# Kernel tuning notes

Measured on AMD Instinct MI355X. Metric: run time of the kernel, lower is better.

Reference implementation:

```python
import jax, jax.numpy as jnp
import numpy as np
import math

D, H, S, B, E, FF = 768, 12, 1024, 2, 32768, 4 * 768
HD = D // H


def layer_norm(x, g, b, eps=1e-5):
    m = jnp.mean(x, axis=-1, keepdims=True)
    v = jnp.mean((x - m) ** 2, axis=-1, keepdims=True)
    return (x - m) / jnp.sqrt(v + eps) * g + b


def setup_inputs() -> dict:
    key = jax.random.key(0)
    ks = jax.random.split(key, 24)
    w = lambda k, shape: jax.random.normal(k, shape, dtype=jnp.float32) * 0.02
    inp = {
        "x": jax.random.normal(ks[0], (B, S, D), dtype=jnp.float32),
        "adj_mask": jax.random.randint(ks[1], (B, S, S), 0, 2).astype(bool),
        "edge_attr": jax.random.normal(ks[2], (E,), dtype=jnp.float32),
        "edge_index": jax.random.randint(ks[3], (2, E), 0, S),
        "norm1_g": jnp.ones((D,), jnp.float32),
        "norm1_b": jnp.zeros((D,), jnp.float32),
        "Wq": w(ks[4], (D, D)), "bq": jnp.zeros((D,), jnp.float32),
        "Wk": w(ks[5], (D, D)), "bk": jnp.zeros((D,), jnp.float32),
        "Wv": w(ks[6], (D, D)), "bv": jnp.zeros((D,), jnp.float32),
        "Wo": w(ks[7], (D, D)), "bo": jnp.zeros((D,), jnp.float32),
        "norm2_g": jnp.ones((D,), jnp.float32),
        "norm2_b": jnp.zeros((D,), jnp.float32),
        "mlp_W1": w(ks[8], (D, FF)), "mlp_b1": jnp.zeros((FF,), jnp.float32),
        "mlp_W2": w(ks[9], (FF, D)), "mlp_b2": jnp.zeros((D,), jnp.float32),
        # per-head edge-attr MLP: Linear(1,16) -> GELU -> Linear(16,1), stacked over H heads
        "ep_W1": w(ks[10], (H, 16)), "ep_b1": jnp.zeros((H, 16), jnp.float32),
        "ep_W2": w(ks[11], (H, 16)), "ep_b2": jnp.zeros((H,), jnp.float32),
    }
    return inp


def reference(x, adj_mask, edge_attr, edge_index,
              norm1_g, norm1_b, Wq, bq, Wk, bk, Wv, bv, Wo, bo,
              norm2_g, norm2_b, mlp_W1, mlp_b1, mlp_W2, mlp_b2,
              ep_W1, ep_b1, ep_W2, ep_b2):
    Bb, Ss, Dd = x.shape
    Hh = ep_W1.shape[0]
    hd = Dd // Hh
    residual = x
    nx = layer_norm(x, norm1_g, norm1_b)
    q = (nx @ Wq + bq).reshape(Bb, Ss, Hh, hd).transpose(0, 2, 1, 3)  # [B,H,S,hd]
    k = (nx @ Wk + bk).reshape(Bb, Ss, Hh, hd).transpose(0, 2, 1, 3)
    v = (nx @ Wv + bv).reshape(Bb, Ss, Hh, hd).transpose(0, 2, 1, 3)
    scores = jnp.einsum('bhqd,bhkd->bhqk', q, k) / math.sqrt(hd)
    mask = adj_mask.astype(bool)[:, None]  # [B,1,S,S]
    scores = jnp.where(mask, scores, jnp.float32(-1e9))
    # per-edge per-head bias (computed under no_grad in the original -> stop_gradient)
    h1 = jax.nn.gelu(edge_attr[:, None, None] * ep_W1[None] + ep_b1[None], approximate=False)  # [E,H,16]
    proj = jnp.einsum('ehk,hk->eh', h1, ep_W2) + ep_b2  # [E,H]
    proj = jax.lax.stop_gradient(proj)
    src, dst = edge_index[0], edge_index[1]
    bias = jnp.zeros((Hh, Ss, Ss), x.dtype).at[:, src, dst].set(proj.T)  # [H,S,S]
    scores = scores + jnp.where(mask, bias[None], jnp.float32(0.0))
    attn = jax.nn.softmax(scores, axis=-1)
    out = jnp.einsum('bhqk,bhkd->bhqd', attn, v)
    out = out.transpose(0, 2, 1, 3).reshape(Bb, Ss, Dd)
    x = residual + (out @ Wo + bo)
    y = layer_norm(x, norm2_g, norm2_b)
    y = jax.nn.gelu(y @ mlp_W1 + mlp_b1, approximate=False) @ mlp_W2 + mlp_b2
    return x + y
```

## Files before the change

kernel.cpp:

```cpp
#include <hip/hip_runtime.h>
#include <hip/hip_bf16.h>

#define B_ 2
#define S_ 1024
#define D_ 768
#define H_ 12
#define HD_ 64
#define FF_ 3072
#define E_ 32768
#define QS_ 2304
#define NSPLIT 2
#define NSPLIT_W2 4
#define BHS (B_ * H_ * S_)

typedef short bf16x8 __attribute__((ext_vector_type(8)));
typedef float f32x4 __attribute__((ext_vector_type(4)));

#define SW(row, seg) ((((seg) ^ ((row) & 7)) * 8))

__device__ __forceinline__ unsigned short f2bf(float f) {
    __hip_bfloat16 h = __float2bfloat16(f);
    return __builtin_bit_cast(unsigned short, h);
}
__device__ __forceinline__ float bf2f(unsigned short u) {
    unsigned int v = ((unsigned int)u) << 16;
    return __builtin_bit_cast(float, v);
}
__device__ __forceinline__ float gelu_exact(float x) {
    return 0.5f * x * (1.0f + erff(x * 0.70710678118654752f));
}
__device__ __forceinline__ void gload_lds16(const unsigned short* g, unsigned short* l) {
    __builtin_amdgcn_global_load_lds((const __attribute__((address_space(1))) void*)g,
                                     (__attribute__((address_space(3))) void*)l, 16, 0, 0);
}

__global__ __launch_bounds__(256) void ln_kernel(
    const float* __restrict__ x, const float* __restrict__ g,
    const float* __restrict__ b, unsigned short* __restrict__ out)
{
    const int row = blockIdx.x;
    const int t = threadIdx.x;
    const float* xr = x + (size_t)row * D_;
    float v0 = xr[t], v1 = xr[t + 256], v2 = xr[t + 512];
    float s = v0 + v1 + v2, s2 = v0 * v0 + v1 * v1 + v2 * v2;
    for (int m = 32; m; m >>= 1) { s += __shfl_xor(s, m); s2 += __shfl_xor(s2, m); }
    __shared__ float red[8];
    const int w = t >> 6;
    if ((t & 63) == 0) { red[w] = s; red[4 + w] = s2; }
    __syncthreads();
    s = red[0] + red[1] + red[2] + red[3];
    s2 = red[4] + red[5] + red[6] + red[7];
    const float mean = s * (1.f / D_);
    const float var = s2 * (1.f / D_) - mean * mean;
    const float rstd = rsqrtf(var + 1e-5f);
    unsigned short* orow = out + (size_t)row * D_;
    orow[t]       = f2bf((v0 - mean) * rstd * g[t]       + b[t]);
    orow[t + 256] = f2bf((v1 - mean) * rstd * g[t + 256] + b[t + 256]);
    orow[t + 512] = f2bf((v2 - mean) * rstd * g[t + 512] + b[t + 512]);
}

__global__ __launch_bounds__(256) void wtrans_all_kernel(
    const float* __restrict__ Wq, const float* __restrict__ Wk, const float* __restrict__ Wv,
    const float* __restrict__ Wo, const float* __restrict__ W1, const float* __restrict__ W2,
    unsigned short* __restrict__ wqkvt, unsigned short* __restrict__ wot,
    unsigned short* __restrict__ w1t, unsigned short* __restrict__ w2t,
    const float* __restrict__ bq, const float* __restrict__ bk, const float* __restrict__ bv,
    float* __restrict__ bqkv)
{
    const int z = blockIdx.z;
    const float* src; unsigned short* dst; int K, N, nb, kb;
    if (z < 4) {
        if (blockIdx.x >= 24 || blockIdx.y >= 24) return;
        K = 768; N = 768; nb = blockIdx.x * 32; kb = blockIdx.y * 32;
        src = (z == 0) ? Wq : (z == 1) ? Wk : (z == 2) ? Wv : Wo;
        dst = (z == 3) ? wot : wqkvt + (size_t)z * 768 * 768;
    } else if (z == 4) {
        if (blockIdx.y >= 24) return;
        K = 768; N = 3072; nb = blockIdx.x * 32; kb = blockIdx.y * 32;
        src = W1; dst = w1t;
    } else {
        if (blockIdx.y >= 24) return;
        K = 3072; N = 768; nb = blockIdx.y * 32; kb = blockIdx.x * 32;
        src = W2; dst = w2t;
    }
    __shared__ float tile[32][33];
    const int tx = threadIdx.x & 31, ty = threadIdx.x >> 5;
    for (int r = 0; r < 32; r += 8)
        tile[ty + r][tx] = src[(size_t)(kb + ty + r) * N + nb + tx];
    __syncthreads();
    for (int r = 0; r < 32; r += 8)
        dst[(size_t)(nb + ty + r) * K + kb + tx] = f2bf(tile[tx][ty + r]);
    if (z == 0 && blockIdx.x == 0 && blockIdx.y == 0) {
        for (int i = threadIdx.x; i < QS_; i += 256)
            bqkv[i] = (i < 768) ? bq[i] : (i < 1536) ? bk[i - 768] : bv[i - 1536];
    }
}

template<bool RES, bool OUTBF>
__global__ __launch_bounds__(256) void gemm_kernel(
    const unsigned short* __restrict__ A, const unsigned short* __restrict__ Bt,
    const float* __restrict__ bias, const float* __restrict__ res,
    void* __restrict__ outp, int M, int N, int K)
{
    __shared__ unsigned short As[64][40];
    __shared__ unsigned short Bs[64][40];
    const int m0 = blockIdx.y * 64, n0 = blockIdx.x * 64;
    const int t = threadIdx.x;
    const int w = t >> 6, l = t & 63;
    const int wm = w >> 1, wn = w & 1;
    const int r = l & 15, g = l >> 4;
    const int srow = t >> 2, sseg = t & 3;
    f32x4 acc[2][2] = {};
    for (int k0 = 0; k0 < K; k0 += 32) {
        __syncthreads();
        const uint4 av = *reinterpret_cast<const uint4*>(A + (size_t)(m0 + srow) * K + k0 + sseg * 8);
        *reinterpret_cast<uint4*>(&As[srow][sseg * 8]) = av;
        const uint4 bv = *reinterpret_cast<const uint4*>(Bt + (size_t)(n0 + srow) * K + k0 + sseg * 8);
        *reinterpret_cast<uint4*>(&Bs[srow][sseg * 8]) = bv;
        __syncthreads();
        bf16x8 af[2], bfr[2];
        af[0]  = *reinterpret_cast<const bf16x8*>(&As[wm * 32 + r][g * 8]);
        af[1]  = *reinterpret_cast<const bf16x8*>(&As[wm * 32 + 16 + r][g * 8]);
        bfr[0] = *reinterpret_cast<const bf16x8*>(&Bs[wn * 32 + r][g * 8]);
        bfr[1] = *reinterpret_cast<const bf16x8*>(&Bs[wn * 32 + 16 + r][g * 8]);
        for (int m = 0; m < 2; m++)
            for (int n = 0; n < 2; n++)
                acc[m][n] = __builtin_amdgcn_mfma_f32_16x16x32_bf16(af[m], bfr[n], acc[m][n], 0, 0, 0);
    }
    for (int m = 0; m < 2; m++)
        for (int n = 0; n < 2; n++) {
            const int col = n0 + wn * 32 + n * 16 + r;
            const float bvv = bias[col];
            for (int j = 0; j < 4; j++) {
                const int row = m0 + wm * 32 + m * 16 + g * 4 + j;
                float v = acc[m][n][j] + bvv;
                if (RES) v += res[(size_t)row * N + col];
                if (OUTBF) ((unsigned short*)outp)[(size_t)row * N + col] = f2bf(v);
                else       ((float*)outp)[(size_t)row * N + col] = v;
            }
        }
}

template<bool GELU, bool OUTBF, bool SPLITK>
__global__ __launch_bounds__(256) void gemm128_kernel(
    const unsigned short* __restrict__ A, const unsigned short* __restrict__ Bt,
    const float* __restrict__ bias, void* __restrict__ outp,
    int M, int N, int K, int klen, int scale_below)
{
    __shared__ unsigned short As[128][64];
    __shared__ unsigned short Bs[128][64];
    const int m0 = blockIdx.y * 128, n0 = blockIdx.x * 128;
    const int t = threadIdx.x;
    const int w = t >> 6, l = t & 63;
    const int wm = w >> 1, wn = w & 1;
    const int lr = l & 15, g = l >> 4;
    const int lrow8 = l >> 3;
    const int lseg = (l & 7) ^ lrow8;
    const int kbeg = SPLITK ? blockIdx.z * klen : 0;
    const int kend = SPLITK ? kbeg + klen : K;
    f32x4 acc[4][4] = {};
    for (int k0 = kbeg; k0 < kend; k0 += 64) {
        __syncthreads();
        for (int j = 0; j < 4; j++) {
            const int q = w * 4 + j;
            const int row = q * 8 + lrow8;
            gload_lds16(A  + (size_t)(m0 + row) * K + k0 + lseg * 8, &As[q * 8][0]);
            gload_lds16(Bt + (size_t)(n0 + row) * K + k0 + lseg * 8, &Bs[q * 8][0]);
        }
        __syncthreads();
        for (int kk = 0; kk < 2; kk++) {
            bf16x8 af[4], bfr[4];
            for (int m = 0; m < 4; m++) {
                const int r = wm * 64 + m * 16 + lr;
                af[m] = *reinterpret_cast<const bf16x8*>(&As[r][SW(r, kk * 4 + g)]);
            }
            for (int n = 0; n < 4; n++) {
                const int r = wn * 64 + n * 16 + lr;
                bfr[n] = *reinterpret_cast<const bf16x8*>(&Bs[r][SW(r, kk * 4 + g)]);
            }
            for (int m = 0; m < 4; m++)
                for (int n = 0; n < 4; n++)
                    acc[m][n] = __builtin_amdgcn_mfma_f32_16x16x32_bf16(af[m], bfr[n], acc[m][n], 0, 0, 0);
        }
    }
    if (SPLITK) {
        float* op = (float*)outp + (size_t)blockIdx.z * M * N;
        for (int m = 0; m < 4; m++)
            for (int n = 0; n < 4; n++) {
                const int col = n0 + wn * 64 + n * 16 + lr;
                for (int j = 0; j < 4; j++) {
                    const int row = m0 + wm * 64 + m * 16 + g * 4 + j;
                    op[(size_t)row * N + col] = acc[m][n][j];
                }
            }
    } else {
        for (int m = 0; m < 4; m++)
            for (int n = 0; n < 4; n++) {
                const int col = n0 + wn * 64 + n * 16 + lr;
                const float scl = (col < scale_below) ? 0.125f : 1.0f;
                const float bvv = bias[col];
                for (int j = 0; j < 4; j++) {
                    const int row = m0 + wm * 64 + m * 16 + g * 4 + j;
                    float v = (acc[m][n][j] + bvv) * scl;
                    if (GELU) v = gelu_exact(v);
                    if (OUTBF) ((unsigned short*)outp)[(size_t)row * N + col] = f2bf(v);
                    else       ((float*)outp)[(size_t)row * N + col] = v;
                }
            }
    }
}

__global__ __launch_bounds__(256) void w2_reduce_kernel(
    const float* __restrict__ part, const float* __restrict__ x2,
    const float* __restrict__ b2, float* __restrict__ out)
{
    const int idx = (blockIdx.x * 256 + threadIdx.x) * 4;
    const int col = idx % D_;
    const float4 xr = *reinterpret_cast<const float4*>(&x2[idx]);
    const float4 bb = *reinterpret_cast<const float4*>(&b2[col]);
    float4 o;
    o.x = xr.x + bb.x; o.y = xr.y + bb.y; o.z = xr.z + bb.z; o.w = xr.w + bb.w;
    for (int s = 0; s < NSPLIT_W2; s++) {
        const float4 p = *reinterpret_cast<const float4*>(&part[(size_t)s * B_ * S_ * D_ + idx]);
        o.x += p.x; o.y += p.y; o.z += p.z; o.w += p.w;
    }
    *reinterpret_cast<float4*>(&out[idx]) = o;
}

__global__ __launch_bounds__(256) void vtrans_kernel(
    const unsigned short* __restrict__ qkv, unsigned short* __restrict__ vt)
{
    __shared__ unsigned short T[64][68];
    const int t = threadIdx.x;
    const int s0 = blockIdx.x * 64;
    const int h = blockIdx.y, b = blockIdx.z;
    const int r = t >> 2, seg = t & 3;
    const unsigned short* src = qkv + (size_t)(b * S_ + s0 + r) * QS_ + 1536 + h * HD_ + seg * 16;
    *reinterpret_cast<uint4*>(&T[r][seg * 16])     = *reinterpret_cast<const uint4*>(src);
    *reinterpret_cast<uint4*>(&T[r][seg * 16 + 8]) = *reinterpret_cast<const uint4*>(src + 8);
    __syncthreads();
    unsigned short tmp[16];
    for (int i = 0; i < 16; i++) tmp[i] = T[seg * 16 + i][r];
    unsigned short* dst = vt + ((size_t)(b * H_ + h) * HD_ + r) * S_ + s0 + seg * 16;
    *reinterpret_cast<uint4*>(dst)     = *reinterpret_cast<uint4*>(&tmp[0]);
    *reinterpret_cast<uint4*>(dst + 8) = *reinterpret_cast<uint4*>(&tmp[8]);
}

__global__ __launch_bounds__(256) void edge_proj_scatter_kernel(
    const float* __restrict__ ea, const float* __restrict__ W1, const float* __restrict__ b1,
    const float* __restrict__ W2, const float* __restrict__ b2,
    const int* __restrict__ ei, float* __restrict__ proj, int* __restrict__ winner)
{
    const int tid = blockIdx.x * 256 + threadIdx.x;
    const int e = tid / H_, h = tid - e * H_;
    const float a = ea[e];
    float s = 0.f;
    for (int j = 0; j < 16; j++) {
        const float tv = a * W1[h * 16 + j] + b1[h * 16 + j];
        s += gelu_exact(tv) * W2[h * 16 + j];
    }
    proj[tid] = s + b2[h];
    if (h == 0) {
        const int sn = ei[e], dn = ei[E_ + e];
        atomicMax(&winner[sn * S_ + dn], e);
    }
}

__global__ __launch_bounds__(256) void ebias_kernel(
    const int* __restrict__ winner, const float* __restrict__ proj,
    unsigned short* __restrict__ ebias)
{
    const int q = blockIdx.x;
    const int t = threadIdx.x;
    const int k4 = t * 4;
    const int4 wv = *reinterpret_cast<const int4*>(&winner[q * S_ + k4]);
    for (int h = 0; h < H_; h++) {
        unsigned int lo = 0, hi = 0;
        if (wv.x >= 0) lo |= (unsigned int)f2bf(proj[(size_t)wv.x * H_ + h]);
        if (wv.y >= 0) lo |= ((unsigned int)f2bf(proj[(size_t)wv.y * H_ + h])) << 16;
        if (wv.z >= 0) hi |= (unsigned int)f2bf(proj[(size_t)wv.z * H_ + h]);
        if (wv.w >= 0) hi |= ((unsigned int)f2bf(proj[(size_t)wv.w * H_ + h])) << 16;
        uint2 val; val.x = lo; val.y = hi;
        *reinterpret_cast<uint2*>(&ebias[((size_t)h * S_ + q) * S_ + k4]) = val;
    }
}

__global__ __launch_bounds__(256) void maskpack_kernel(
    const void* __restrict__ adj, unsigned int* __restrict__ mp, int* __restrict__ winner)
{
    const int q = blockIdx.x, b = blockIdx.y;
    const int t = threadIdx.x;
    if (b == 0) {
        int4 v; v.x = -1; v.y = -1; v.z = -1; v.w = -1;
        reinterpret_cast<int4*>(winner)[q * 256 + t] = v;
    }
    __shared__ unsigned int words[32];
    __shared__ int u8f;
    if (t < 32) words[t] = 0;
    if (t == 0) u8f = 0;
    __syncthreads();
    const unsigned int* row8 = (const unsigned int*)((const unsigned char*)adj + ((size_t)b * S_ + q) * S_);
    const unsigned int* row32 = (const unsigned int*)((const int*)adj + ((size_t)b * S_ + q) * S_);
    const unsigned int v = row8[t];
    if (v & 0xFF00FF00u) atomicOr(&u8f, 1);
    __syncthreads();
    if (u8f) {
        unsigned int nib = 0;
        if (v & 0x000000FFu) nib |= 1u;
        if (v & 0x0000FF00u) nib |= 2u;
        if (v & 0x00FF0000u) nib |= 4u;
        if (v & 0xFF000000u) nib |= 8u;
        if (nib) atomicOr(&words[t >> 3], nib << ((t & 7) * 4));
    } else {
        for (int i = 0; i < 4; i++) {
            const int k = i * 256 + t;
            if (row32[k]) atomicOr(&words[k >> 5], 1u << (k & 31));
        }
    }
    __syncthreads();
    if (t < 32) mp[((size_t)b * S_ + q) * 32 + t] = words[t];
}

__global__ __launch_bounds__(256) void attn_mfma_kernel(
    const unsigned short* __restrict__ qkv,
    const unsigned short* __restrict__ vt,
    const unsigned short* __restrict__ ebias,
    const unsigned int* __restrict__ mp,
    float* __restrict__ pacc,
    float2* __restrict__ pml)
{
    __shared__ unsigned short Ks[64][64];
    __shared__ unsigned short Vs[64][64];
    __shared__ unsigned short Eb[64][72];
    __shared__ unsigned int   Mw[64][2];
    __shared__ unsigned short Ps[4][16][64];
    const int t = threadIdx.x;
    const int w = t >> 6, l = t & 63;
    const int lr = l & 15, g = l >> 4;
    const int qt = blockIdx.x & 15, sp = blockIdx.x >> 4;
    const int q0 = qt * 64;
    const int h = blockIdx.y, b = blockIdx.z;
    const int bh = b * H_ + h;
    const size_t qbase = (size_t)b * S_ * QS_ + h * HD_;
    const size_t kbase = qbase + 768;
    const size_t vtbase = (size_t)bh * HD_ * S_;

    const int qrow = q0 + w * 16 + lr;
    const bf16x8 af0 = *reinterpret_cast<const bf16x8*>(qkv + qbase + (size_t)qrow * QS_ + g * 8);
    const bf16x8 af1 = *reinterpret_cast<const bf16x8*>(qkv + qbase + (size_t)qrow * QS_ + 32 + g * 8);

    float m_run[4], l_run[4];
    f32x4 acc[4] = {};
    for (int j = 0; j < 4; j++) { m_run[j] = -3.0e38f; l_run[j] = 0.f; }

    const int srow = t >> 2, sseg = t & 3;
    const int kt_beg = sp * (S_ / NSPLIT), kt_end = kt_beg + S_ / NSPLIT;
    for (int kt = kt_beg; kt < kt_end; kt += 64) {
        __syncthreads();
        {
            const unsigned short* ksrc = qkv + kbase + (size_t)(kt + srow) * QS_ + sseg * 16;
            *reinterpret_cast<uint4*>(&Ks[srow][SW(srow, sseg * 2)])     = *reinterpret_cast<const uint4*>(ksrc);
            *reinterpret_cast<uint4*>(&Ks[srow][SW(srow, sseg * 2 + 1)]) = *reinterpret_cast<const uint4*>(ksrc + 8);
            const unsigned short* vsrc = vt + vtbase + (size_t)srow * S_ + kt + sseg * 16;
            *reinterpret_cast<uint4*>(&Vs[srow][SW(srow, sseg * 2)])     = *reinterpret_cast<const uint4*>(vsrc);
            *reinterpret_cast<uint4*>(&Vs[srow][SW(srow, sseg * 2 + 1)]) = *reinterpret_cast<const uint4*>(vsrc + 8);
            const unsigned short* esrc = ebias + ((size_t)h * S_ + q0 + srow) * S_ + kt + sseg * 16;
            *reinterpret_cast<uint4*>(&Eb[srow][sseg * 16])     = *reinterpret_cast<const uint4*>(esrc);
            *reinterpret_cast<uint4*>(&Eb[srow][sseg * 16 + 8]) = *reinterpret_cast<const uint4*>(esrc + 8);
            if (t < 128) Mw[t >> 1][t & 1] = mp[((size_t)b * S_ + q0 + (t >> 1)) * 32 + (kt >> 5) + (t & 1)];
        }
        __syncthreads();
        f32x4 sc[4];
        for (int n = 0; n < 4; n++) {
            const int r = n * 16 + lr;
            const bf16x8 b0 = *reinterpret_cast<const bf16x8*>(&Ks[r][SW(r, g)]);
            const bf16x8 b1 = *reinterpret_cast<const bf16x8*>(&Ks[r][SW(r, 4 + g)]);
            f32x4 z = {};
            z = __builtin_amdgcn_mfma_f32_16x16x32_bf16(af0, b0, z, 0, 0, 0);
            z = __builtin_amdgcn_mfma_f32_16x16x32_bf16(af1, b1, z, 0, 0, 0);
            sc[n] = z;
        }
        float tmax[4] = {-3.0e38f, -3.0e38f, -3.0e38f, -3.0e38f};
        for (int n = 0; n < 4; n++) {
            for (int j = 0; j < 4; j++) {
                const int rq = w * 16 + g * 4 + j;
                const unsigned int word = Mw[rq][n >> 1];
                const bool msk = (word >> ((n & 1) * 16 + lr)) & 1;
                float sval;
                if (msk) sval = sc[n][j] + bf2f(Eb[rq][n * 16 + lr]);
                else sval = -1e9f;
                sc[n][j] = sval;
                tmax[j] = fmaxf(tmax[j], sval);
            }
        }
        float pscale[4];
        for (int j = 0; j < 4; j++) {
            float tm = tmax[j];
            tm = fmaxf(tm, __shfl_xor(tm, 1));
            tm = fmaxf(tm, __shfl_xor(tm, 2));
            tm = fmaxf(tm, __shfl_xor(tm, 4));
            tm = fmaxf(tm, __shfl_xor(tm, 8));
            const float mnew = fmaxf(m_run[j], tm);
            pscale[j] = __expf(m_run[j] - mnew);
            m_run[j] = mnew;
            l_run[j] *= pscale[j];
        }
        float psum[4] = {0.f, 0.f, 0.f, 0.f};
        for (int n = 0; n < 4; n++) {
            for (int j = 0; j < 4; j++) {
                const float p = __expf(sc[n][j] - m_run[j]);
                psum[j] += p;
                const int row = g * 4 + j;
                Ps[w][row][SW(row, n * 2 + (lr >> 3)) + (lr & 7)] = f2bf(p);
            }
        }
        for (int j = 0; j < 4; j++) {
            float s = psum[j];
            s += __shfl_xor(s, 1); s += __shfl_xor(s, 2);
            s += __shfl_xor(s, 4); s += __shfl_xor(s, 8);
            l_run[j] += s;
            for (int n2 = 0; n2 < 4; n2++) acc[n2][j] *= pscale[j];
        }
        const bf16x8 pa0 = *reinterpret_cast<const bf16x8*>(&Ps[w][lr][SW(lr, g)]);
        const bf16x8 pa1 = *reinterpret_cast<const bf16x8*>(&Ps[w][lr][SW(lr, 4 + g)]);
        for (int n2 = 0; n2 < 4; n2++) {
            const int r = n2 * 16 + lr;
            const bf16x8 vb0 = *reinterpret_cast<const bf16x8*>(&Vs[r][SW(r, g)]);
            const bf16x8 vb1 = *reinterpret_cast<const bf16x8*>(&Vs[r][SW(r, 4 + g)]);
            acc[n2] = __builtin_amdgcn_mfma_f32_16x16x32_bf16(pa0, vb0, acc[n2], 0, 0, 0);
            acc[n2] = __builtin_amdgcn_mfma_f32_16x16x32_bf16(pa1, vb1, acc[n2], 0, 0, 0);
        }
    }
    const size_t prow = (size_t)sp * BHS + (size_t)bh * S_;
    for (int j = 0; j < 4; j++) {
        const int qg = q0 + w * 16 + g * 4 + j;
        for (int n2 = 0; n2 < 4; n2++)
            pacc[(prow + qg) * 64 + n2 * 16 + lr] = acc[n2][j];
        if (lr == 0) { float2 v; v.x = m_run[j]; v.y = l_run[j]; pml[prow + qg] = v; }
    }
}

__global__ __launch_bounds__(256) void attn_combine_kernel(
    const float* __restrict__ pacc, const float2* __restrict__ pml,
    unsigned short* __restrict__ attnb)
{
    const int idx = (blockIdx.x * 256 + threadIdx.x) * 4;
    const int r = idx >> 6, d = idx & 63;
    float2 ml[NSPLIT];
    float mx = -3.0e38f;
    for (int s = 0; s < NSPLIT; s++) {
        ml[s] = pml[(size_t)s * BHS + r];
        mx = fmaxf(mx, ml[s].x);
    }
    float wgt[NSPLIT], L = 0.f;
    for (int s = 0; s < NSPLIT; s++) {
        wgt[s] = __expf(ml[s].x - mx);
        L += ml[s].y * wgt[s];
    }
    const float inv = (L > 0.f) ? 1.f / L : 0.f;
    float4 o = {0.f, 0.f, 0.f, 0.f};
    for (int s = 0; s < NSPLIT; s++) {
        const float4 a = *reinterpret_cast<const float4*>(&pacc[((size_t)s * BHS + r) * 64 + d]);
        o.x += a.x * wgt[s]; o.y += a.y * wgt[s];
        o.z += a.z * wgt[s]; o.w += a.w * wgt[s];
    }
    const int bh = r >> 10, q = r & 1023;
    const int b = bh / H_, h = bh - b * H_;
    ushort4 ov;
    ov.x = f2bf(o.x * inv); ov.y = f2bf(o.y * inv);
    ov.z = f2bf(o.z * inv); ov.w = f2bf(o.w * inv);
    *reinterpret_cast<ushort4*>(&attnb[((size_t)(b * S_ + q)) * D_ + h * HD_ + d]) = ov;
}

extern "C" void kernel_launch(void* const* d_in, const int* in_sizes, int n_in,
                              void* d_out, int out_size, void* d_ws, size_t ws_size,
                              hipStream_t stream)
{
    const float* x    = (const float*)d_in[0];
    const void*  adj  = d_in[1];
    const float* ea   = (const float*)d_in[2];
    const int*   ei   = (const int*)d_in[3];
    const float* g1   = (const float*)d_in[4];
    const float* bn1  = (const float*)d_in[5];
    const float* Wq   = (const float*)d_in[6];
    const float* bq   = (const float*)d_in[7];
    const float* Wk   = (const float*)d_in[8];
    const float* bk   = (const float*)d_in[9];
    const float* Wv   = (const float*)d_in[10];
    const float* bv   = (const float*)d_in[11];
    const float* Wo   = (const float*)d_in[12];
    const float* bo   = (const float*)d_in[13];
    const float* g2   = (const float*)d_in[14];
    const float* bn2  = (const float*)d_in[15];
    const float* W1   = (const float*)d_in[16];
    const float* mb1  = (const float*)d_in[17];
    const float* W2   = (const float*)d_in[18];
    const float* mb2  = (const float*)d_in[19];
    const float* epW1 = (const float*)d_in[20];
    const float* epb1 = (const float*)d_in[21];
    const float* epW2 = (const float*)d_in[22];
    const float* epb2 = (const float*)d_in[23];

    char* ws = (char*)d_ws;
    size_t off = 0;
    auto carve = [&](size_t bytes) -> void* {
        void* p = ws + off;
        off += (bytes + 255) & ~(size_t)255;
        return p;
    };
    unsigned short* wqkvt = (unsigned short*)carve((size_t)QS_ * D_ * 2);
    unsigned short* wot   = (unsigned short*)carve((size_t)D_ * D_ * 2);
    unsigned short* w1t   = (unsigned short*)carve((size_t)FF_ * D_ * 2);
    unsigned short* w2t   = (unsigned short*)carve((size_t)D_ * FF_ * 2);
    float*          bqkv  = (float*)carve((size_t)QS_ * 4);
    float*          proj  = (float*)carve((size_t)E_ * H_ * 4);
    int*            winner= (int*)carve((size_t)S_ * S_ * 4);
    unsigned short* ebias = (unsigned short*)carve((size_t)H_ * S_ * S_ * 2);
    unsigned int*   mpk   = (unsigned int*)carve((size_t)B_ * S_ * 32 * 4);
    unsigned short* nxb   = (unsigned short*)carve((size_t)B_ * S_ * D_ * 2);
    unsigned short* attnb = (unsigned short*)carve((size_t)B_ * S_ * D_ * 2);
    unsigned short* qkv   = (unsigned short*)carve((size_t)B_ * S_ * QS_ * 2);
    unsigned short* vtb   = (unsigned short*)carve((size_t)B_ * S_ * D_ * 2);
    float*          x2f   = (float*)carve((size_t)B_ * S_ * D_ * 4);
    float*          pacc  = (float*)carve((size_t)NSPLIT * BHS * 64 * 4);
    float2*         pml   = (float2*)carve((size_t)NSPLIT * BHS * 8);
    unsigned short* ln2b = nxb;
    unsigned short* hb   = qkv;
    float*          pw2  = (float*)ebias;

    const int M = B_ * S_;

    maskpack_kernel<<<dim3(S_, B_), 256, 0, stream>>>(adj, mpk, winner);

    wtrans_all_kernel<<<dim3(96, 24, 6), 256, 0, stream>>>(
        Wq, Wk, Wv, Wo, W1, W2, wqkvt, wot, w1t, w2t, bq, bk, bv, bqkv);

    ln_kernel<<<M, 256, 0, stream>>>(x, g1, bn1, nxb);

    gemm128_kernel<false, true, false><<<dim3(QS_ / 128, M / 128), 256, 0, stream>>>(
        nxb, wqkvt, bqkv, qkv, M, QS_, D_, D_, 768);

    vtrans_kernel<<<dim3(S_ / 64, H_, B_), 256, 0, stream>>>(qkv, vtb);

    edge_proj_scatter_kernel<<<(E_ * H_) / 256, 256, 0, stream>>>(
        ea, epW1, epb1, epW2, epb2, ei, proj, winner);
    ebias_kernel<<<S_, 256, 0, stream>>>(winner, proj, ebias);

    attn_mfma_kernel<<<dim3(16 * NSPLIT, H_, B_), 256, 0, stream>>>(
        qkv, vtb, ebias, mpk, pacc, pml);
    attn_combine_kernel<<<(BHS * 64) / 1024, 256, 0, stream>>>(pacc, pml, attnb);

    gemm_kernel<true, false><<<dim3(D_ / 64, M / 64), 256, 0, stream>>>(
        attnb, wot, bo, x, x2f, M, D_, D_);

    ln_kernel<<<M, 256, 0, stream>>>(x2f, g2, bn2, ln2b);

    gemm128_kernel<true, true, false><<<dim3(FF_ / 128, M / 128), 256, 0, stream>>>(
        ln2b, w1t, mb1, hb, M, FF_, D_, D_, 0);
    gemm128_kernel<false, false, true><<<dim3(D_ / 128, M / 128, NSPLIT_W2), 256, 0, stream>>>(
        hb, w2t, mb2, pw2, M, D_, FF_, FF_ / NSPLIT_W2, 0);
    w2_reduce_kernel<<<(M * D_) / 1024, 256, 0, stream>>>(pw2, x2f, mb2, (float*)d_out);
}
```

Before: 191.1 us.

## Fuse prep kernels, merge V-transpose with edge bias, store split partials in bf16

Maskpack, weight transpose and the first layernorm are merged into one flat-grid prep kernel, and the V transpose and edge-bias build are merged into one mid kernel, cutting the number of launches. Attention KV splits go from 2 to 4 to give more blocks in the grid. Attention partial accumulators and the split-K W2 partials are now stored in bf16 instead of fp32, halving that intermediate traffic. The bf16 partials lose precision in the reductions, and the extra splits add combine work.

```diff
diff --git a/kernel.cpp b/kernel.cpp
--- a/kernel.cpp
+++ b/kernel.cpp
@@ -9,7 +9,7 @@
 #define FF_ 3072
 #define E_ 32768
 #define QS_ 2304
-#define NSPLIT 2
+#define NSPLIT 4
 #define NSPLIT_W2 4
 #define BHS (B_ * H_ * S_)
 
@@ -32,6 +32,101 @@
 __device__ __forceinline__ void gload_lds16(const unsigned short* g, unsigned short* l) {
     __builtin_amdgcn_global_load_lds((const __attribute__((address_space(1))) void*)g,
                                      (__attribute__((address_space(3))) void*)l, 16, 0, 0);
+}
+
+__global__ __launch_bounds__(256) void prep_kernel(
+    const void* __restrict__ adj, unsigned int* __restrict__ mp, int* __restrict__ winner,
+    const float* __restrict__ Wq, const float* __restrict__ Wk, const float* __restrict__ Wv,
+    const float* __restrict__ Wo, const float* __restrict__ W1, const float* __restrict__ W2,
+    unsigned short* __restrict__ wqkvt, unsigned short* __restrict__ wot,
+    unsigned short* __restrict__ w1t, unsigned short* __restrict__ w2t,
+    const float* __restrict__ bq, const float* __restrict__ bk, const float* __restrict__ bv,
+    float* __restrict__ bqkv,
+    const float* __restrict__ x, const float* __restrict__ g1, const float* __restrict__ bn1,
+    unsigned short* __restrict__ nxb)
+{
+    __shared__ float tile[32][33];
+    __shared__ unsigned int words[32];
+    __shared__ int u8f;
+    __shared__ float red[8];
+    const int blk = blockIdx.x;
+    const int t = threadIdx.x;
+
+    if (blk < 2048) {
+        const int b = blk >> 10, q = blk & 1023;
+        if (b == 0) {
+            int4 v; v.x = -1; v.y = -1; v.z = -1; v.w = -1;
+            reinterpret_cast<int4*>(winner)[q * 256 + t] = v;
+        }
+        if (t < 32) words[t] = 0;
+        if (t == 0) u8f = 0;
+        __syncthreads();
+        const unsigned int* row8 = (const unsigned int*)((const unsigned char*)adj + ((size_t)b * S_ + q) * S_);
+        const unsigned int* row32 = (const unsigned int*)((const int*)adj + ((size_t)b * S_ + q) * S_);
+        const unsigned int v = row8[t];
+        if (v & 0xFF00FF00u) atomicOr(&u8f, 1);
+        __syncthreads();
+        if (u8f) {
+            unsigned int nib = 0;
+            if (v & 0x000000FFu) nib |= 1u;
+            if (v & 0x0000FF00u) nib |= 2u;
+            if (v & 0x00FF0000u) nib |= 4u;
+            if (v & 0xFF000000u) nib |= 8u;
+            if (nib) atomicOr(&words[t >> 3], nib << ((t & 7) * 4));
+        } else {
+            for (int i = 0; i < 4; i++) {
+                const int k = i * 256 + t;
+                if (row32[k]) atomicOr(&words[k >> 5], 1u << (k & 31));
+            }
+        }
+        __syncthreads();
+        if (t < 32) mp[((size_t)b * S_ + q) * 32 + t] = words[t];
+    } else if (blk < 8960) {
+        const int w = blk - 2048;
+        const float* src; unsigned short* dst; int K, N, nb, kb;
+        if (w < 2304) {
+            const int z = w / 576, r = w - z * 576;
+            K = 768; N = 768; kb = (r / 24) * 32; nb = (r % 24) * 32;
+            src = (z == 0) ? Wq : (z == 1) ? Wk : (z == 2) ? Wv : Wo;
+            dst = (z == 3) ? wot : wqkvt + (size_t)z * 768 * 768;
+        } else if (w < 4608) {
+            const int r = w - 2304;
+            K = 768; N = 3072; nb = (r % 96) * 32; kb = (r / 96) * 32;
+            src = W1; dst = w1t;
+        } else {
+            const int r = w - 4608;
+            K = 3072; N = 768; kb = (r % 96) * 32; nb = (r / 96) * 32;
+            src = W2; dst = w2t;
+        }
+        const int tx = t & 31, ty = t >> 5;
+        for (int r = 0; r < 32; r += 8)
+            tile[ty + r][tx] = src[(size_t)(kb + ty + r) * N + nb + tx];
+        __syncthreads();
+        for (int r = 0; r < 32; r += 8)
+            dst[(size_t)(nb + ty + r) * K + kb + tx] = f2bf(tile[tx][ty + r]);
+        if (w == 0) {
+            for (int i = t; i < QS_; i += 256)
+                bqkv[i] = (i < 768) ? bq[i] : (i < 1536) ? bk[i - 768] : bv[i - 1536];
+        }
+    } else {
+        const int row = blk - 8960;
+        const float* xr = x + (size_t)row * D_;
+        float v0 = xr[t], v1 = xr[t + 256], v2 = xr[t + 512];
+        float s = v0 + v1 + v2, s2 = v0 * v0 + v1 * v1 + v2 * v2;
+        for (int m = 32; m; m >>= 1) { s += __shfl_xor(s, m); s2 += __shfl_xor(s2, m); }
+        const int w = t >> 6;
+        if ((t & 63) == 0) { red[w] = s; red[4 + w] = s2; }
+        __syncthreads();
+        s = red[0] + red[1] + red[2] + red[3];
+        s2 = red[4] + red[5] + red[6] + red[7];
+        const float mean = s * (1.f / D_);
+        const float var = s2 * (1.f / D_) - mean * mean;
+        const float rstd = rsqrtf(var + 1e-5f);
+        unsigned short* orow = nxb + (size_t)row * D_;
+        orow[t]       = f2bf((v0 - mean) * rstd * g1[t]       + bn1[t]);
+        orow[t + 256] = f2bf((v1 - mean) * rstd * g1[t + 256] + bn1[t + 256]);
+        orow[t + 512] = f2bf((v2 - mean) * rstd * g1[t + 512] + bn1[t + 512]);
+    }
 }
 
 __global__ __launch_bounds__(256) void ln_kernel(
@@ -59,40 +154,61 @@
     orow[t + 512] = f2bf((v2 - mean) * rstd * g[t + 512] + b[t + 512]);
 }
 
-__global__ __launch_bounds__(256) void wtrans_all_kernel(
-    const float* __restrict__ Wq, const float* __restrict__ Wk, const float* __restrict__ Wv,
-    const float* __restrict__ Wo, const float* __restrict__ W1, const float* __restrict__ W2,
-    unsigned short* __restrict__ wqkvt, unsigned short* __restrict__ wot,
-    unsigned short* __restrict__ w1t, unsigned short* __restrict__ w2t,
-    const float* __restrict__ bq, const float* __restrict__ bk, const float* __restrict__ bv,
-    float* __restrict__ bqkv)
-{
-    const int z = blockIdx.z;
-    const float* src; unsigned short* dst; int K, N, nb, kb;
-    if (z < 4) {
-        if (blockIdx.x >= 24 || blockIdx.y >= 24) return;
-        K = 768; N = 768; nb = blockIdx.x * 32; kb = blockIdx.y * 32;
-        src = (z == 0) ? Wq : (z == 1) ? Wk : (z == 2) ? Wv : Wo;
-        dst = (z == 3) ? wot : wqkvt + (size_t)z * 768 * 768;
-    } else if (z == 4) {
-        if (blockIdx.y >= 24) return;
-        K = 768; N = 3072; nb = blockIdx.x * 32; kb = blockIdx.y * 32;
-        src = W1; dst = w1t;
+__global__ __launch_bounds__(256) void edge_proj_scatter_kernel(
+    const float* __restrict__ ea, const float* __restrict__ W1, const float* __restrict__ b1,
+    const float* __restrict__ W2, const float* __restrict__ b2,
+    const int* __restrict__ ei, float* __restrict__ proj, int* __restrict__ winner)
+{
+    const int tid = blockIdx.x * 256 + threadIdx.x;
+    const int e = tid / H_, h = tid - e * H_;
+    const float a = ea[e];
+    float s = 0.f;
+    for (int j = 0; j < 16; j++) {
+        const float tv = a * W1[h * 16 + j] + b1[h * 16 + j];
+        s += gelu_exact(tv) * W2[h * 16 + j];
+    }
+    proj[tid] = s + b2[h];
+    if (h == 0) {
+        const int sn = ei[e], dn = ei[E_ + e];
+        atomicMax(&winner[sn * S_ + dn], e);
+    }
+}
+
+__global__ __launch_bounds__(256) void mid_kernel(
+    const unsigned short* __restrict__ qkv, unsigned short* __restrict__ vt,
+    const int* __restrict__ winner, const float* __restrict__ proj,
+    unsigned short* __restrict__ ebias)
+{
+    __shared__ unsigned short T[64][68];
+    const int blk = blockIdx.x;
+    const int t = threadIdx.x;
+    if (blk < 384) {
+        const int s0 = (blk & 15) * 64;
+        const int rest = blk >> 4;
+        const int h = rest % 12, b = rest / 12;
+        const int r = t >> 2, seg = t & 3;
+        const unsigned short* src = qkv + (size_t)(b * S_ + s0 + r) * QS_ + 1536 + h * HD_ + seg * 16;
+        *reinterpret_cast<uint4*>(&T[r][seg * 16])     = *reinterpret_cast<const uint4*>(src);
+        *reinterpret_cast<uint4*>(&T[r][seg * 16 + 8]) = *reinterpret_cast<const uint4*>(src + 8);
+        __syncthreads();
+        unsigned short tmp[16];
+        for (int i = 0; i < 16; i++) tmp[i] = T[seg * 16 + i][r];
+        unsigned short* dst = vt + ((size_t)(b * H_ + h) * HD_ + r) * S_ + s0 + seg * 16;
+        *reinterpret_cast<uint4*>(dst)     = *reinterpret_cast<uint4*>(&tmp[0]);
+        *reinterpret_cast<uint4*>(dst + 8) = *reinterpret_cast<uint4*>(&tmp[8]);
     } else {
-        if (blockIdx.y >= 24) return;
-        K = 3072; N = 768; nb = blockIdx.y * 32; kb = blockIdx.x * 32;
-        src = W2; dst = w2t;
-    }
-    __shared__ float tile[32][33];
-    const int tx = threadIdx.x & 31, ty = threadIdx.x >> 5;
-    for (int r = 0; r < 32; r += 8)
-        tile[ty + r][tx] = src[(size_t)(kb + ty + r) * N + nb + tx];
-    __syncthreads();
-    for (int r = 0; r < 32; r += 8)
-        dst[(size_t)(nb + ty + r) * K + kb + tx] = f2bf(tile[tx][ty + r]);
-    if (z == 0 && blockIdx.x == 0 && blockIdx.y == 0) {
-        for (int i = threadIdx.x; i < QS_; i += 256)
-            bqkv[i] = (i < 768) ? bq[i] : (i < 1536) ? bk[i - 768] : bv[i - 1536];
+        const int q = blk - 384;
+        const int k4 = t * 4;
+        const int4 wv = *reinterpret_cast<const int4*>(&winner[q * S_ + k4]);
+        for (int h = 0; h < H_; h++) {
+            unsigned int lo = 0, hi = 0;
+            if (wv.x >= 0) lo |= (unsigned int)f2bf(proj[(size_t)wv.x * H_ + h]);
+            if (wv.y >= 0) lo |= ((unsigned int)f2bf(proj[(size_t)wv.y * H_ + h])) << 16;
+            if (wv.z >= 0) hi |= (unsigned int)f2bf(proj[(size_t)wv.z * H_ + h]);
+            if (wv.w >= 0) hi |= ((unsigned int)f2bf(proj[(size_t)wv.w * H_ + h])) << 16;
+            uint2 val; val.x = lo; val.y = hi;
+            *reinterpret_cast<uint2*>(&ebias[((size_t)h * S_ + q) * S_ + k4]) = val;
+        }
     }
 }
 
@@ -184,13 +300,13 @@
         }
     }
     if (SPLITK) {
-        float* op = (float*)outp + (size_t)blockIdx.z * M * N;
         for (int m = 0; m < 4; m++)
             for (int n = 0; n < 4; n++) {
                 const int col = n0 + wn * 64 + n * 16 + lr;
                 for (int j = 0; j < 4; j++) {
                     const int row = m0 + wm * 64 + m * 16 + g * 4 + j;
-                    op[(size_t)row * N + col] = acc[m][n][j];
+                    if (OUTBF) ((unsigned short*)outp)[((size_t)blockIdx.z * M + row) * N + col] = f2bf(acc[m][n][j]);
+                    else       ((float*)outp)[((size_t)blockIdx.z * M + row) * N + col] = acc[m][n][j];
                 }
             }
     } else {
@@ -211,7 +327,7 @@
 }
 
 __global__ __launch_bounds__(256) void w2_reduce_kernel(
-    const float* __restrict__ part, const float* __restrict__ x2,
+    const unsigned short* __restrict__ part, const float* __restrict__ x2,
     const float* __restrict__ b2, float* __restrict__ out)
 {
     const int idx = (blockIdx.x * 256 + threadIdx.x) * 4;
@@ -221,104 +337,13 @@
     float4 o;
     o.x = xr.x + bb.x; o.y = xr.y + bb.y; o.z = xr.z + bb.z; o.w = xr.w + bb.w;
     for (int s = 0; s < NSPLIT_W2; s++) {
-        const float4 p = *reinterpret_cast<const float4*>(&part[(size_t)s * B_ * S_ * D_ + idx]);
-        o.x += p.x; o.y += p.y; o.z += p.z; o.w += p.w;
+        const uint2 p = *reinterpret_cast<const uint2*>(&part[(size_t)s * B_ * S_ * D_ + idx]);
+        o.x += bf2f((unsigned short)(p.x & 0xFFFF));
+        o.y += bf2f((unsigned short)(p.x >> 16));
+        o.z += bf2f((unsigned short)(p.y & 0xFFFF));
+        o.w += bf2f((unsigned short)(p.y >> 16));
     }
     *reinterpret_cast<float4*>(&out[idx]) = o;
-}
-
-__global__ __launch_bounds__(256) void vtrans_kernel(
-    const unsigned short* __restrict__ qkv, unsigned short* __restrict__ vt)
-{
-    __shared__ unsigned short T[64][68];
-    const int t = threadIdx.x;
-    const int s0 = blockIdx.x * 64;
-    const int h = blockIdx.y, b = blockIdx.z;
-    const int r = t >> 2, seg = t & 3;
-    const unsigned short* src = qkv + (size_t)(b * S_ + s0 + r) * QS_ + 1536 + h * HD_ + seg * 16;
-    *reinterpret_cast<uint4*>(&T[r][seg * 16])     = *reinterpret_cast<const uint4*>(src);
-    *reinterpret_cast<uint4*>(&T[r][seg * 16 + 8]) = *reinterpret_cast<const uint4*>(src + 8);
-    __syncthreads();
-    unsigned short tmp[16];
-    for (int i = 0; i < 16; i++) tmp[i] = T[seg * 16 + i][r];
-    unsigned short* dst = vt + ((size_t)(b * H_ + h) * HD_ + r) * S_ + s0 + seg * 16;
-    *reinterpret_cast<uint4*>(dst)     = *reinterpret_cast<uint4*>(&tmp[0]);
-    *reinterpret_cast<uint4*>(dst + 8) = *reinterpret_cast<uint4*>(&tmp[8]);
-}
-
-__global__ __launch_bounds__(256) void edge_proj_scatter_kernel(
-    const float* __restrict__ ea, const float* __restrict__ W1, const float* __restrict__ b1,
-    const float* __restrict__ W2, const float* __restrict__ b2,
-    const int* __restrict__ ei, float* __restrict__ proj, int* __restrict__ winner)
-{
-    const int tid = blockIdx.x * 256 + threadIdx.x;
-    const int e = tid / H_, h = tid - e * H_;
-    const float a = ea[e];
-    float s = 0.f;
-    for (int j = 0; j < 16; j++) {
-        const float tv = a * W1[h * 16 + j] + b1[h * 16 + j];
-        s += gelu_exact(tv) * W2[h * 16 + j];
-    }
-    proj[tid] = s + b2[h];
-    if (h == 0) {
-        const int sn = ei[e], dn = ei[E_ + e];
-        atomicMax(&winner[sn * S_ + dn], e);
-    }
-}
-
-__global__ __launch_bounds__(256) void ebias_kernel(
-    const int* __restrict__ winner, const float* __restrict__ proj,
-    unsigned short* __restrict__ ebias)
-{
-    const int q = blockIdx.x;
-    const int t = threadIdx.x;
-    const int k4 = t * 4;
-    const int4 wv = *reinterpret_cast<const int4*>(&winner[q * S_ + k4]);
-    for (int h = 0; h < H_; h++) {
-        unsigned int lo = 0, hi = 0;
-        if (wv.x >= 0) lo |= (unsigned int)f2bf(proj[(size_t)wv.x * H_ + h]);
-        if (wv.y >= 0) lo |= ((unsigned int)f2bf(proj[(size_t)wv.y * H_ + h])) << 16;
-        if (wv.z >= 0) hi |= (unsigned int)f2bf(proj[(size_t)wv.z * H_ + h]);
-        if (wv.w >= 0) hi |= ((unsigned int)f2bf(proj[(size_t)wv.w * H_ + h])) << 16;
-        uint2 val; val.x = lo; val.y = hi;
-        *reinterpret_cast<uint2*>(&ebias[((size_t)h * S_ + q) * S_ + k4]) = val;
-    }
-}
-
-__global__ __launch_bounds__(256) void maskpack_kernel(
-    const void* __restrict__ adj, unsigned int* __restrict__ mp, int* __restrict__ winner)
-{
-    const int q = blockIdx.x, b = blockIdx.y;
-    const int t = threadIdx.x;
-    if (b == 0) {
-        int4 v; v.x = -1; v.y = -1; v.z = -1; v.w = -1;
-        reinterpret_cast<int4*>(winner)[q * 256 + t] = v;
-    }
-    __shared__ unsigned int words[32];
-    __shared__ int u8f;
-    if (t < 32) words[t] = 0;
-    if (t == 0) u8f = 0;
-    __syncthreads();
-    const unsigned int* row8 = (const unsigned int*)((const unsigned char*)adj + ((size_t)b * S_ + q) * S_);
-    const unsigned int* row32 = (const unsigned int*)((const int*)adj + ((size_t)b * S_ + q) * S_);
-    const unsigned int v = row8[t];
-    if (v & 0xFF00FF00u) atomicOr(&u8f, 1);
-    __syncthreads();
-    if (u8f) {
-        unsigned int nib = 0;
-        if (v & 0x000000FFu) nib |= 1u;
-        if (v & 0x0000FF00u) nib |= 2u;
-        if (v & 0x00FF0000u) nib |= 4u;
-        if (v & 0xFF000000u) nib |= 8u;
-        if (nib) atomicOr(&words[t >> 3], nib << ((t & 7) * 4));
-    } else {
-        for (int i = 0; i < 4; i++) {
-            const int k = i * 256 + t;
-            if (row32[k]) atomicOr(&words[k >> 5], 1u << (k & 31));
-        }
-    }
-    __syncthreads();
-    if (t < 32) mp[((size_t)b * S_ + q) * 32 + t] = words[t];
 }
 
 __global__ __launch_bounds__(256) void attn_mfma_kernel(
@@ -326,7 +351,7 @@
     const unsigned short* __restrict__ vt,
     const unsigned short* __restrict__ ebias,
     const unsigned int* __restrict__ mp,
-    float* __restrict__ pacc,
+    unsigned short* __restrict__ pacc,
     float2* __restrict__ pml)
 {
     __shared__ unsigned short Ks[64][64];
@@ -435,13 +460,13 @@
     for (int j = 0; j < 4; j++) {
         const int qg = q0 + w * 16 + g * 4 + j;
         for (int n2 = 0; n2 < 4; n2++)
-            pacc[(prow + qg) * 64 + n2 * 16 + lr] = acc[n2][j];
+            pacc[(prow + qg) * 64 + n2 * 16 + lr] = f2bf(acc[n2][j]);
         if (lr == 0) { float2 v; v.x = m_run[j]; v.y = l_run[j]; pml[prow + qg] = v; }
     }
 }
 
 __global__ __launch_bounds__(256) void attn_combine_kernel(
-    const float* __restrict__ pacc, const float2* __restrict__ pml,
+    const unsigned short* __restrict__ pacc, const float2* __restrict__ pml,
     unsigned short* __restrict__ attnb)
 {
     const int idx = (blockIdx.x * 256 + threadIdx.x) * 4;
@@ -460,9 +485,11 @@
     const float inv = (L > 0.f) ? 1.f / L : 0.f;
     float4 o = {0.f, 0.f, 0.f, 0.f};
     for (int s = 0; s < NSPLIT; s++) {
-        const float4 a = *reinterpret_cast<const float4*>(&pacc[((size_t)s * BHS + r) * 64 + d]);
-        o.x += a.x * wgt[s]; o.y += a.y * wgt[s];
-        o.z += a.z * wgt[s]; o.w += a.w * wgt[s];
+        const uint2 p = *reinterpret_cast<const uint2*>(&pacc[((size_t)s * BHS + r) * 64 + d]);
+        o.x += bf2f((unsigned short)(p.x & 0xFFFF)) * wgt[s];
+        o.y += bf2f((unsigned short)(p.x >> 16)) * wgt[s];
+        o.z += bf2f((unsigned short)(p.y & 0xFFFF)) * wgt[s];
+        o.w += bf2f((unsigned short)(p.y >> 16)) * wgt[s];
     }
     const int bh = r >> 10, q = r & 1023;
     const int b = bh / H_, h = bh - b * H_;
@@ -522,29 +549,26 @@
     unsigned short* qkv   = (unsigned short*)carve((size_t)B_ * S_ * QS_ * 2);
     unsigned short* vtb   = (unsigned short*)carve((size_t)B_ * S_ * D_ * 2);
     float*          x2f   = (float*)carve((size_t)B_ * S_ * D_ * 4);
-    float*          pacc  = (float*)carve((size_t)NSPLIT * BHS * 64 * 4);
+    unsigned short* pacc  = (unsigned short*)carve((size_t)NSPLIT * BHS * 64 * 2);
     float2*         pml   = (float2*)carve((size_t)NSPLIT * BHS * 8);
     unsigned short* ln2b = nxb;
     unsigned short* hb   = qkv;
-    float*          pw2  = (float*)ebias;
+    unsigned short* pw2  = (unsigned short*)ebias;
 
     const int M = B_ * S_;
 
-    maskpack_kernel<<<dim3(S_, B_), 256, 0, stream>>>(adj, mpk, winner);
-
-    wtrans_all_kernel<<<dim3(96, 24, 6), 256, 0, stream>>>(
-        Wq, Wk, Wv, Wo, W1, W2, wqkvt, wot, w1t, w2t, bq, bk, bv, bqkv);
-
-    ln_kernel<<<M, 256, 0, stream>>>(x, g1, bn1, nxb);
+    prep_kernel<<<11008, 256, 0, stream>>>(
+        adj, mpk, winner,
+        Wq, Wk, Wv, Wo, W1, W2, wqkvt, wot, w1t, w2t, bq, bk, bv, bqkv,
+        x, g1, bn1, nxb);
+
+    edge_proj_scatter_kernel<<<(E_ * H_) / 256, 256, 0, stream>>>(
+        ea, epW1, epb1, epW2, epb2, ei, proj, winner);
 
     gemm128_kernel<false, true, false><<<dim3(QS_ / 128, M / 128), 256, 0, stream>>>(
         nxb, wqkvt, bqkv, qkv, M, QS_, D_, D_, 768);
 
-    vtrans_kernel<<<dim3(S_ / 64, H_, B_), 256, 0, stream>>>(qkv, vtb);
-
-    edge_proj_scatter_kernel<<<(E_ * H_) / 256, 256, 0, stream>>>(
-        ea, epW1, epb1, epW2, epb2, ei, proj, winner);
-    ebias_kernel<<<S_, 256, 0, stream>>>(winner, proj, ebias);
+    mid_kernel<<<384 + S_, 256, 0, stream>>>(qkv, vtb, winner, proj, ebias);
 
     attn_mfma_kernel<<<dim3(16 * NSPLIT, H_, B_), 256, 0, stream>>>(
         qkv, vtb, ebias, mpk, pacc, pml);
@@ -557,7 +581,7 @@
 
     gemm128_kernel<true, true, false><<<dim3(FF_ / 128, M / 128), 256, 0, stream>>>(
         ln2b, w1t, mb1, hb, M, FF_, D_, D_, 0);
-    gemm128_kernel<false, false, true><<<dim3(D_ / 128, M / 128, NSPLIT_W2), 256, 0, stream>>>(
+    gemm128_kernel<false, true, true><<<dim3(D_ / 128, M / 128, NSPLIT_W2), 256, 0, stream>>>(
         hb, w2t, mb2, pw2, M, D_, FF_, FF_ / NSPLIT_W2, 0);
     w2_reduce_kernel<<<(M * D_) / 1024, 256, 0, stream>>>(pw2, x2f, mb2, (float*)d_out);
 }
```

New measurement: 182.3 us. 1.05x faster.
